# Performance work log

Measured on AMD Instinct MI355X. Metric: run time of the kernel, lower is better.

## Reference

```python
import jax, jax.numpy as jnp
import numpy as np

VOCAB, E, H, OUT = 50000, 300, 512, 256
D = 2 * H  # bidirectional
B, T = 64, 256
EPS = 1e-5


def setup_inputs() -> dict:
    key = jax.random.key(0)
    ks = jax.random.split(key, 16)
    s = 0.05
    inp = {
        'inputs': jax.random.randint(ks[0], (B, T), 0, VOCAB, dtype=jnp.int32),
        'mask': jnp.zeros((B, T), dtype=bool),
        'embed_table': jax.random.normal(ks[1], (VOCAB, E), jnp.float32) * s,
        # forward-direction LSTM (PyTorch gate order i,f,g,o)
        'w_ih_f': jax.random.normal(ks[2], (4 * H, E), jnp.float32) * s,
        'w_hh_f': jax.random.normal(ks[3], (4 * H, H), jnp.float32) * s,
        'b_ih_f': jax.random.normal(ks[4], (4 * H,), jnp.float32) * s,
        'b_hh_f': jax.random.normal(ks[5], (4 * H,), jnp.float32) * s,
        # backward-direction LSTM
        'w_ih_b': jax.random.normal(ks[6], (4 * H, E), jnp.float32) * s,
        'w_hh_b': jax.random.normal(ks[7], (4 * H, H), jnp.float32) * s,
        'b_ih_b': jax.random.normal(ks[8], (4 * H,), jnp.float32) * s,
        'b_hh_b': jax.random.normal(ks[9], (4 * H,), jnp.float32) * s,
        # SoftDotAttention
        'w_in': jax.random.normal(ks[10], (D, D), jnp.float32) * s,       # linear_in, no bias
        'w_out_attn': jax.random.normal(ks[11], (D, 2 * D), jnp.float32) * s,  # linear_out, no bias
        # output head + BatchNorm affine
        'w_out': jax.random.normal(ks[12], (OUT, D), jnp.float32) * s,
        'b_out': jax.random.normal(ks[13], (OUT,), jnp.float32) * s,
        'gamma': jnp.ones((OUT,), jnp.float32),
        'beta': jnp.zeros((OUT,), jnp.float32),
    }
    return inp


def _lstm_dir(x, w_ih, w_hh, b_ih, b_hh, reverse):
    # x: [B, T, E] -> hs: [B, T, H]
    bsz = x.shape[0]
    h0 = jnp.zeros((bsz, w_hh.shape[1]), x.dtype)
    c0 = jnp.zeros_like(h0)
    x_pre = jnp.einsum('bte,ge->btg', x, w_ih) + (b_ih + b_hh)  # precompute input proj

    def cell(carry, xt):
        h, c = carry
        gates = xt + h @ w_hh.T
        i, f, g, o = jnp.split(gates, 4, axis=-1)
        i, f, o = jax.nn.sigmoid(i), jax.nn.sigmoid(f), jax.nn.sigmoid(o)
        g = jnp.tanh(g)
        c = f * c + i * g
        h = o * jnp.tanh(c)
        return (h, c), h

    _, hs = jax.lax.scan(cell, (h0, c0), jnp.swapaxes(x_pre, 0, 1), reverse=reverse)
    return jnp.swapaxes(hs, 0, 1)


def reference(inputs, mask, embed_table, w_ih_f, w_hh_f, b_ih_f, b_hh_f,
              w_ih_b, w_hh_b, b_ih_b, b_hh_b, w_in, w_out_attn,
              w_out, b_out, gamma, beta):
    embeds = embed_table[inputs]                       # [B,T,E]; dropout = identity (eval)
    h_f = _lstm_dir(embeds, w_ih_f, w_hh_f, b_ih_f, b_hh_f, reverse=False)
    h_b = _lstm_dir(embeds, w_ih_b, w_hh_b, b_ih_b, b_hh_b, reverse=True)
    ctx = jnp.concatenate([h_f, h_b], axis=-1)         # [B,T,D]

    # vectorized SoftDotAttention over all query timesteps (the original Python loop)
    target = jnp.einsum('bqd,ed->bqe', ctx, w_in)      # linear_in(ctx[:,q])
    scores = jnp.einsum('bqd,bkd->bqk', target, ctx)   # [B,T,T]
    scores = jnp.where(mask[:, None, :], -jnp.inf, scores)
    attn = jax.nn.softmax(scores, axis=-1)
    weighted = jnp.einsum('bqk,bkd->bqd', attn, ctx)   # [B,T,D]
    h_tilde = jnp.tanh(jnp.einsum('bqc,dc->bqd',
                                  jnp.concatenate([weighted, ctx], axis=-1),
                                  w_out_attn))          # [B,T,D]

    ctx_out = jnp.mean(h_tilde, axis=1)                # [B,D]
    y = jnp.tanh(ctx_out @ w_out.T + b_out)            # [B,OUT]

    # BatchNorm1d, training-mode batch statistics (biased variance)
    mu = jnp.mean(y, axis=0)
    var = jnp.mean((y - mu) ** 2, axis=0)
    out = gamma * (y - mu) * jax.lax.rsqrt(var + EPS) + beta
    return out
```

## Files before the change

### kernel.cpp

```cpp
#include <hip/hip_runtime.h>
#include <hip/hip_fp16.h>

#define NB   64
#define NT   256
#define NE   300
#define NH   512
#define ND   1024
#define NOUT 256

typedef _Float16 f16;
typedef _Float16 f16x4 __attribute__((ext_vector_type(4)));
typedef _Float16 f16x8 __attribute__((ext_vector_type(8)));
typedef float    f32x4 __attribute__((ext_vector_type(4)));

static __device__ __forceinline__ float sigmoidf_(float x) {
  return 1.f / (1.f + __expf(-x));
}
static __device__ __forceinline__ float tanhf_(float x) {
  return 1.f - 2.f / (__expf(2.f * x) + 1.f);
}

template <bool DUAL>
static __device__ __forceinline__ void mfma_tile(
    const f16* __restrict__ A, const f16* __restrict__ A2,
    const f16* __restrict__ B, int K, int Ksplit, int ldA, int ldB,
    int m0, int n0, f32x4 acc[4], f16* As, f16* Bs)
{
  const int tid = threadIdx.x;
  const int lane = tid & 63, w = tid >> 6;
  const int sr = tid >> 2, sk = (tid & 3) * 8;
  const int afr = (w * 16 + (lane & 15)) * 40 + (lane >> 4) * 8;
  for (int kt = 0; kt < K; kt += 32) {
    const f16* Ab = (!DUAL || kt < Ksplit)
        ? (A  + (size_t)(m0 + sr) * ldA + kt + sk)
        : (A2 + (size_t)(m0 + sr) * ldA + (kt - Ksplit) + sk);
    *(f16x8*)&As[sr * 40 + sk] = *(const f16x8*)Ab;
    *(f16x8*)&Bs[sr * 40 + sk] =
        *(const f16x8*)&B[(size_t)(n0 + sr) * ldB + kt + sk];
    __syncthreads();
    f16x8 a = *(const f16x8*)&As[afr];
#pragma unroll
    for (int j = 0; j < 4; ++j) {
      f16x8 b = *(const f16x8*)&Bs[(j * 16 + (lane & 15)) * 40 + (lane >> 4) * 8];
      acc[j] = __builtin_amdgcn_mfma_f32_16x16x32_f16(a, b, acc[j], 0, 0, 0);
    }
    __syncthreads();
  }
}

__global__ __launch_bounds__(256) void gemm_h2h(
    const f16* __restrict__ A, const f16* __restrict__ B, f16* __restrict__ C,
    int N, int K, int sA, int sB, int sC)
{
  __shared__ f16 As[2560], Bs[2560];
  const f16* Ab = A + (size_t)blockIdx.z * sA;
  const f16* Bb = B + (size_t)blockIdx.z * sB;
  f16*       Cb = C + (size_t)blockIdx.z * sC;
  const int m0 = blockIdx.y * 64, n0 = blockIdx.x * 64;
  f32x4 acc[4] = {};
  mfma_tile<false>(Ab, Ab, Bb, K, K, K, K, m0, n0, acc, As, Bs);
  const int lane = threadIdx.x & 63, w = threadIdx.x >> 6;
  const int row = m0 + w * 16 + (lane >> 4) * 4;
  const int col = n0 + (lane & 15);
#pragma unroll
  for (int j = 0; j < 4; ++j)
#pragma unroll
    for (int r = 0; r < 4; ++r)
      Cb[(size_t)(row + r) * N + col + j * 16] = (f16)acc[j][r];
}

__global__ __launch_bounds__(256) void gemm_h2f(
    const f16* __restrict__ A, const f16* __restrict__ B, float* __restrict__ C,
    int N, int K, int sA, int sB, int sC)
{
  __shared__ f16 As[2560], Bs[2560];
  const f16* Ab = A + (size_t)blockIdx.z * sA;
  const f16* Bb = B + (size_t)blockIdx.z * sB;
  float*     Cb = C + (size_t)blockIdx.z * sC;
  const int m0 = blockIdx.y * 64, n0 = blockIdx.x * 64;
  f32x4 acc[4] = {};
  mfma_tile<false>(Ab, Ab, Bb, K, K, K, K, m0, n0, acc, As, Bs);
  const int lane = threadIdx.x & 63, w = threadIdx.x >> 6;
  const int row = m0 + w * 16 + (lane >> 4) * 4;
  const int col = n0 + (lane & 15);
#pragma unroll
  for (int j = 0; j < 4; ++j)
#pragma unroll
    for (int r = 0; r < 4; ++r)
      Cb[(size_t)(row + r) * N + col + j * 16] = acc[j][r];
}

__global__ __launch_bounds__(256) void xpre_mfma(
    const f16* __restrict__ A, const f16* __restrict__ B,
    const float* __restrict__ bihf, const float* __restrict__ bhhf,
    const float* __restrict__ bihb, const float* __restrict__ bhhb,
    f16* __restrict__ xq)
{
  __shared__ __align__(16) f16 As[2560], Bs[2560];
  __shared__ __align__(16) f16 ldsT[64 * 72];
  __shared__ float biasS[64];
  const int ds = blockIdx.x;
  const int dir = ds >> 5, slice = ds & 31;
  const int t0 = blockIdx.y;
  const int tid = threadIdx.x, lane = tid & 63, w = tid >> 6;
  if (tid < 64) {
    int row = dir * 2048 + (tid & 3) * 512 + slice * 16 + (tid >> 2);
    biasS[tid] = (row < 2048) ? (bihf[row] + bhhf[row])
                              : (bihb[row - 2048] + bhhb[row - 2048]);
  }
  const int sr = tid >> 2, sk = (tid & 3) * 8;
  const int brow = dir * 2048 + (sr & 3) * 512 + slice * 16 + (sr >> 2);
  const int afr = (w * 16 + (lane & 15)) * 40 + (lane >> 4) * 8;
  f32x4 acc[4] = {};
  for (int kt = 0; kt < 320; kt += 32) {
    *(f16x8*)&As[sr * 40 + sk] =
        *(const f16x8*)&A[((size_t)(sr * 256 + t0)) * 320 + kt + sk];
    *(f16x8*)&Bs[sr * 40 + sk] =
        *(const f16x8*)&B[((size_t)brow) * 320 + kt + sk];
    __syncthreads();
    f16x8 a = *(const f16x8*)&As[afr];
#pragma unroll
    for (int j = 0; j < 4; ++j) {
      f16x8 b = *(const f16x8*)&Bs[(j * 16 + (lane & 15)) * 40 + (lane >> 4) * 8];
      acc[j] = __builtin_amdgcn_mfma_f32_16x16x32_f16(a, b, acc[j], 0, 0, 0);
    }
    __syncthreads();
  }
#pragma unroll
  for (int j = 0; j < 4; ++j) {
    const int cl = j * 16 + (lane & 15);
#pragma unroll
    for (int r = 0; r < 4; ++r) {
      int b = w * 16 + (lane >> 4) * 4 + r;
      ldsT[b * 72 + cl] = (f16)(acc[j][r] + biasS[cl]);
    }
  }
  __syncthreads();
  f16* base = xq + (((size_t)t0 * 2 + dir) * 32 + slice) * 4096;
#pragma unroll
  for (int p = 0; p < 2; ++p) {
    int e = tid + 256 * p;
    int b = e >> 3, q8 = (e & 7) * 8;
    *(uint4*)(base + b * 64 + q8) = *(const uint4*)&ldsT[b * 72 + q8];
  }
}

__global__ __launch_bounds__(256) void htilde_mfma(
    const f16* __restrict__ Wt, const f16* __restrict__ CTX,
    const f16* __restrict__ Wo, float* __restrict__ ctx_out)
{
  __shared__ f16 As[2560], Bs[2560];
  __shared__ float red[4][64];
  const int m0 = blockIdx.y * 64, n0 = blockIdx.x * 64;
  f32x4 acc[4] = {};
  mfma_tile<true>(Wt, CTX, Wo, 2048, 1024, 1024, 2048, m0, n0, acc, As, Bs);
  const int lane = threadIdx.x & 63, w = threadIdx.x >> 6;
#pragma unroll
  for (int j = 0; j < 4; ++j) {
    float s = 0.f;
#pragma unroll
    for (int r = 0; r < 4; ++r) s += tanhf(acc[j][r]);
    s += __shfl_xor(s, 16, 64);
    s += __shfl_xor(s, 32, 64);
    if (lane < 16) red[w][j * 16 + lane] = s;
  }
  __syncthreads();
  if (threadIdx.x < 64) {
    float s = red[0][threadIdx.x] + red[1][threadIdx.x] +
              red[2][threadIdx.x] + red[3][threadIdx.x];
    int b = m0 >> 8;
    atomicAdd(&ctx_out[(size_t)b * ND + n0 + threadIdx.x], s);
  }
}

__global__ __launch_bounds__(256, 1) void lstm_persist(
    const f16* __restrict__ xq, const float* __restrict__ whhf,
    const float* __restrict__ whhb, f16* __restrict__ hseq)
{
  __shared__ __align__(16) f16 hx[64][24];
  const int blk = blockIdx.x;
  const int dir = blk >> 5;
  const int slice = blk & 31;
  const int j0 = slice * 16;
  const float* whh = dir ? whhb : whhf;
  const int tid = threadIdx.x, lane = tid & 63, w = tid >> 6;
  const int jj = lane & 15, ko = (lane >> 4) * 8;

  f16x8 bf[4][16];
#pragma unroll
  for (int g = 0; g < 4; ++g)
#pragma unroll
    for (int kt = 0; kt < 16; ++kt) {
      const float* src = whh + (size_t)(g * NH + j0 + jj) * NH + kt * 32 + ko;
      float4 u0 = *(const float4*)src;
      float4 u1 = *(const float4*)(src + 4);
      f16x8 v;
      v[0] = (f16)u0.x; v[1] = (f16)u0.y; v[2] = (f16)u0.z; v[3] = (f16)u0.w;
      v[4] = (f16)u1.x; v[5] = (f16)u1.y; v[6] = (f16)u1.z; v[7] = (f16)u1.w;
      bf[g][kt] = v;
    }

  float c[4] = {0.f, 0.f, 0.f, 0.f};
  const int eb = tid >> 2, eg = tid & 3;
  const int aoff = (ko >> 4) * 1024 + (w * 16 + jj) * 16 + (ko & 8);

  float xg[4][4];
  auto ldxg = [&](int t) {
    const int tl = dir ? (NT - 1 - t) : t;
    const f16* base = xq + (((size_t)tl * 2 + dir) * 32 + slice) * 4096;
#pragma unroll
    for (int r = 0; r < 4; ++r) {
      const int b = w * 16 + (lane >> 4) * 4 + r;
      unsigned long long u = *(const unsigned long long*)(base + b * 64 + jj * 4);
      f16x4 x = __builtin_bit_cast(f16x4, u);
      xg[0][r] = (float)x[0];
      xg[1][r] = (float)x[1];
      xg[2][r] = (float)x[2];
      xg[3][r] = (float)x[3];
    }
  };
  ldxg(0);

  unsigned long long u0[16], u1[16];

  for (int t = 0; t < NT; ++t) {
    const int tt = dir ? (NT - 1 - t) : t;

    f32x4 acc[4] = {};
    if (t > 0) {
      const int ttp = dir ? (NT - t) : (t - 1);
      const f16* hp = hseq + ((size_t)ttp * 2 + dir) * 32768 + aoff;
      for (;;) {
        int nb = 0;
#pragma unroll
        for (int kt = 0; kt < 16; ++kt) {
          nb |= (unsigned)(u0[kt] >> 48) == 0xFFFFu;
          nb |= (unsigned)(u1[kt] >> 48) == 0xFFFFu;
        }
        if (!__any(nb)) break;
#pragma unroll
        for (int kt = 0; kt < 16; ++kt) {
          if ((unsigned)(u0[kt] >> 48) == 0xFFFFu)
            u0[kt] = __hip_atomic_load(
                (const unsigned long long*)(hp + kt * 2048),
                __ATOMIC_RELAXED, __HIP_MEMORY_SCOPE_AGENT);
          if ((unsigned)(u1[kt] >> 48) == 0xFFFFu)
            u1[kt] = __hip_atomic_load(
                (const unsigned long long*)(hp + kt * 2048 + 4),
                __ATOMIC_RELAXED, __HIP_MEMORY_SCOPE_AGENT);
        }
      }
#pragma unroll
      for (int kt = 0; kt < 16; ++kt) {
        f16x4 a0 = __builtin_bit_cast(f16x4, u0[kt]);
        f16x4 a1 = __builtin_bit_cast(f16x4, u1[kt]);
        f16x8 a = __builtin_shufflevector(a0, a1, 0, 1, 2, 3, 4, 5, 6, 7);
#pragma unroll
        for (int g = 0; g < 4; ++g)
          acc[g] = __builtin_amdgcn_mfma_f32_16x16x32_f16(a, bf[g][kt], acc[g], 0, 0, 0);
      }
    }
#pragma unroll
    for (int r = 0; r < 4; ++r) {
      float iv = sigmoidf_(acc[0][r] + xg[0][r]);
      float fv = sigmoidf_(acc[1][r] + xg[1][r]);
      float gv = tanhf_   (acc[2][r] + xg[2][r]);
      float ov = sigmoidf_(acc[3][r] + xg[3][r]);
      c[r] = fv * c[r] + iv * gv;
      float h = ov * tanhf_(c[r]);
      hx[w * 16 + (lane >> 4) * 4 + r][jj] = (f16)h;
    }
    asm volatile("s_waitcnt lgkmcnt(0)" ::: "memory");
    __builtin_amdgcn_sched_barrier(0);
    f16x4 hv = *(const f16x4*)&hx[eb][eg * 4];
    unsigned long long pu = __builtin_bit_cast(unsigned long long, hv);
    __hip_atomic_store(
        (unsigned long long*)(hseq + ((size_t)tt * 2 + dir) * 32768
                              + (size_t)slice * 1024 + eb * 16 + eg * 4),
        pu, __ATOMIC_RELAXED, __HIP_MEMORY_SCOPE_AGENT);
    if (t == NT - 1) break;
    {
      const f16* hn = hseq + ((size_t)tt * 2 + dir) * 32768 + aoff;
#pragma unroll
      for (int kt = 0; kt < 16; ++kt) {
        u0[kt] = __hip_atomic_load(
            (const unsigned long long*)(hn + kt * 2048),
            __ATOMIC_RELAXED, __HIP_MEMORY_SCOPE_AGENT);
        u1[kt] = __hip_atomic_load(
            (const unsigned long long*)(hn + kt * 2048 + 4),
            __ATOMIC_RELAXED, __HIP_MEMORY_SCOPE_AGENT);
      }
    }
    ldxg(t + 1);
  }
}

__global__ __launch_bounds__(256) void fill_sent(unsigned long long* __restrict__ p)
{
  size_t i = (size_t)blockIdx.x * 1024 + threadIdx.x;
#pragma unroll
  for (int k = 0; k < 4; ++k)
    __hip_atomic_store(p + i + k * 256, 0xFFFFFFFFFFFFFFFFull,
                       __ATOMIC_RELAXED, __HIP_MEMORY_SCOPE_AGENT);
}

__global__ __launch_bounds__(256) void tr_k(
    const f16* __restrict__ hseq, f16* __restrict__ ctx, f16* __restrict__ ctxT)
{
  __shared__ __align__(16) f16 X[4][64][72];
  const int t0 = blockIdx.x * 64;
  const int dir = blockIdx.y;
  const int bg = blockIdx.z;
  const int tid = threadIdx.x;
  for (int ci = 0; ci < 8; ++ci) {
#pragma unroll
    for (int p = 0; p < 8; ++p) {
      int q = tid + 256 * p;
      int ti = q >> 5, rem = q & 31;
      int si = rem >> 3, s2 = rem & 7;
      int bi = s2 >> 1, jjh = (s2 & 1) * 8;
      const f16* src = hseq
          + (((size_t)(t0 + ti) * 2 + dir) * 32 + ci * 4 + si) * 1024
          + (bg * 4 + bi) * 16 + jjh;
      *(uint4*)&X[bi][ti][si * 16 + jjh] = *(const uint4*)src;
    }
    __syncthreads();
#pragma unroll
    for (int p = 0; p < 8; ++p) {
      int q = tid + 256 * p;
      int bi = q >> 9, rem = q & 511;
      int ti = rem >> 3, sub = (rem & 7) * 8;
      f16* dst = ctx + ((size_t)(bg * 4 + bi) * NT + t0 + ti) * ND
                 + dir * 512 + ci * 64 + sub;
      *(uint4*)dst = *(const uint4*)&X[bi][ti][sub];
    }
#pragma unroll
    for (int p = 0; p < 8; ++p) {
      int q = tid + 256 * p;
      int bi = q >> 9, rem = q & 511;
      int dl = rem >> 3, ts = (rem & 7) * 8;
      f16x8 v;
#pragma unroll
      for (int k = 0; k < 8; ++k) v[k] = X[bi][ts + k][dl];
      f16* dst = ctxT + ((size_t)(bg * 4 + bi) * ND + dir * 512 + ci * 64 + dl) * NT
                 + t0 + ts;
      *(f16x8*)dst = v;
    }
    __syncthreads();
  }
}

__global__ __launch_bounds__(256) void softmax_rows(
    const float* __restrict__ sc, f16* __restrict__ probs)
{
  const int row = blockIdx.x * 4 + (threadIdx.x >> 6);
  const int lane = threadIdx.x & 63;
  const float* p = sc + (size_t)row * NT;
  float4 v = *(const float4*)&p[lane * 4];
  float mx = fmaxf(fmaxf(v.x, v.y), fmaxf(v.z, v.w));
#pragma unroll
  for (int s = 32; s >= 1; s >>= 1) mx = fmaxf(mx, __shfl_xor(mx, s, 64));
  v.x = __expf(v.x - mx); v.y = __expf(v.y - mx);
  v.z = __expf(v.z - mx); v.w = __expf(v.w - mx);
  float sm = v.x + v.y + v.z + v.w;
#pragma unroll
  for (int s = 32; s >= 1; s >>= 1) sm += __shfl_xor(sm, s, 64);
  float inv = 1.f / sm;
  f16* q = probs + (size_t)row * NT + lane * 4;
  q[0] = (f16)(v.x * inv); q[1] = (f16)(v.y * inv);
  q[2] = (f16)(v.z * inv); q[3] = (f16)(v.w * inv);
}

__global__ __launch_bounds__(256) void head_k(
    const float* __restrict__ ctx_out, const float* __restrict__ w_out,
    const float* __restrict__ b_out, float* __restrict__ y)
{
  const int b = blockIdx.x;
  __shared__ float cl[ND];
#pragma unroll
  for (int l = 0; l < 4; ++l)
    cl[threadIdx.x + 256 * l] =
        ctx_out[(size_t)b * ND + threadIdx.x + 256 * l] * (1.f / (float)NT);
  __syncthreads();
  const int n = threadIdx.x;
  float acc = b_out[n];
  for (int k = 0; k < ND; k += 4) {
    float4 w = *(const float4*)&w_out[(size_t)n * ND + k];
    acc += cl[k] * w.x + cl[k + 1] * w.y + cl[k + 2] * w.z + cl[k + 3] * w.w;
  }
  y[b * NOUT + n] = tanhf(acc);
}

__global__ __launch_bounds__(64) void bn_k(
    const float* __restrict__ y, const float* __restrict__ gamma,
    const float* __restrict__ beta, float* __restrict__ out)
{
  const int n = blockIdx.x, b = threadIdx.x;
  float v = y[b * NOUT + n];
  float s = v, sq = v * v;
#pragma unroll
  for (int k = 32; k >= 1; k >>= 1) {
    s  += __shfl_xor(s, k, 64);
    sq += __shfl_xor(sq, k, 64);
  }
  float mu = s * (1.f / 64.f);
  float var = sq * (1.f / 64.f) - mu * mu;
  float r = rsqrtf(var + 1e-5f);
  out[b * NOUT + n] = gamma[n] * (v - mu) * r + beta[n];
}

__global__ __launch_bounds__(256) void zero_k(float4* __restrict__ p, int n4)
{
  int i = blockIdx.x * 256 + threadIdx.x;
  if (i < n4) p[i] = make_float4(0.f, 0.f, 0.f, 0.f);
}

__global__ __launch_bounds__(256) void gather_emb(
    const int* __restrict__ toks, const float* __restrict__ table,
    f16* __restrict__ emb)
{
  const int w = threadIdx.x >> 6, lane = threadIdx.x & 63;
  const int row = blockIdx.x * 4 + w;
  const int tok = toks[row];
  for (int k = lane; k < 320; k += 64)
    emb[(size_t)row * 320 + k] = (k < NE) ? (f16)table[(size_t)tok * NE + k]
                                          : (f16)0.f;
}

__global__ __launch_bounds__(256) void cvt_wih(
    const float* __restrict__ wf, const float* __restrict__ wb,
    f16* __restrict__ o)
{
  const int row = blockIdx.x;
  const float* src = (row < 2048) ? (wf + (size_t)row * NE)
                                  : (wb + (size_t)(row - 2048) * NE);
  for (int k = threadIdx.x; k < 320; k += 256)
    o[(size_t)row * 320 + k] = (k < NE) ? (f16)src[k] : (f16)0.f;
}

__global__ __launch_bounds__(256) void cvt_flat(
    const float* __restrict__ in, f16* __restrict__ o, int n)
{
  int i = blockIdx.x * 256 + threadIdx.x;
  if (i < n) o[i] = (f16)in[i];
}

extern "C" void kernel_launch(void* const* d_in, const int* in_sizes, int n_in,
                              void* d_out, int out_size, void* d_ws,
                              size_t ws_size, hipStream_t stream)
{
  (void)in_sizes; (void)n_in; (void)out_size;
  const int*   inputs  = (const int*)d_in[0];
  const float* table   = (const float*)d_in[2];
  const float* w_ih_f  = (const float*)d_in[3];
  const float* w_hh_f  = (const float*)d_in[4];
  const float* b_ih_f  = (const float*)d_in[5];
  const float* b_hh_f  = (const float*)d_in[6];
  const float* w_ih_b  = (const float*)d_in[7];
  const float* w_hh_b  = (const float*)d_in[8];
  const float* b_ih_b  = (const float*)d_in[9];
  const float* b_hh_b  = (const float*)d_in[10];
  const float* w_in    = (const float*)d_in[11];
  const float* w_oattn = (const float*)d_in[12];
  const float* w_out   = (const float*)d_in[13];
  const float* b_out   = (const float*)d_in[14];
  const float* gamma   = (const float*)d_in[15];
  const float* beta    = (const float*)d_in[16];

  char* ws = (char*)d_ws;
  f16*   xq      = (f16*)ws;
  f16*   ctxT_h  = (f16*)ws;
  f16*   tw_h    = (f16*)(ws + 33554432);
  float* scores  = (float*)(ws + 67108864);
  f16*   probs   = (f16*)(ws + 83886080);
  f16*   w_in_h  = (f16*)(ws + 92274688);
  f16*   ctx_h   = (f16*)(ws + 134217728);
  f16*   hseq    = (f16*)(ws + 167772160);
  f16*   emb_h   = (f16*)(ws + 201326592);
  float* ctxout  = (float*)(ws + 201588736);
  float* yb      = (float*)(ws + 201850880);
  f16*   wih_h   = (f16*)(ws + 211812352);
  f16*   w_oattn_h = (f16*)(ws + 214433792);
  if (ws_size < 218628096ULL) return;

  gather_emb<<<4096, 256, 0, stream>>>(inputs, table, emb_h);
  cvt_wih<<<4096, 256, 0, stream>>>(w_ih_f, w_ih_b, wih_h);
  cvt_flat<<<8192, 256, 0, stream>>>(w_oattn, w_oattn_h, 2097152);

  fill_sent<<<4096, 256, 0, stream>>>((unsigned long long*)hseq);

  xpre_mfma<<<dim3(64, 256), 256, 0, stream>>>(
      emb_h, wih_h, b_ih_f, b_hh_f, b_ih_b, b_hh_b, xq);

  zero_k<<<82, 256, 0, stream>>>((float4*)ctxout, 20992);
  lstm_persist<<<64, 256, 0, stream>>>(xq, w_hh_f, w_hh_b, hseq);

  tr_k<<<dim3(4, 2, 16), 256, 0, stream>>>(hseq, ctx_h, ctxT_h);

  cvt_flat<<<4096, 256, 0, stream>>>(w_in, w_in_h, 1048576);
  gemm_h2h<<<dim3(16, 256, 1), 256, 0, stream>>>(
      ctx_h, w_in_h, tw_h, ND, ND, 0, 0, 0);

  gemm_h2f<<<dim3(4, 4, NB), 256, 0, stream>>>(
      tw_h, ctx_h, scores, NT, ND, NT * ND, NT * ND, NT * NT);

  softmax_rows<<<(NB * NT) / 4, 256, 0, stream>>>(scores, probs);

  gemm_h2h<<<dim3(16, 4, NB), 256, 0, stream>>>(
      probs, ctxT_h, tw_h, ND, NT, NT * NT, ND * NT, NT * ND);

  htilde_mfma<<<dim3(16, 256), 256, 0, stream>>>(tw_h, ctx_h, w_oattn_h, ctxout);

  head_k<<<NB, 256, 0, stream>>>(ctxout, w_out, b_out, yb);

  bn_k<<<NOUT, 64, 0, stream>>>(yb, gamma, beta, (float*)d_out);
}
```

Before: 1.713 ms.

## Use 128-bit sc1 loads/stores and per-tile incremental MFMA in LSTM recurrence polling

The cross-block exchange of LSTM hidden states now uses 16-byte inline-asm global loads and stores with the sc1 cache bit, replacing pairs of 8-byte relaxed atomic loads and 8-byte atomic stores. The spin-wait no longer waits for the whole h vector before computing. It tracks which k-tiles have arrived (sentinel-checked across the wave) and issues their MFMAs at once, re-polling only the missing tiles. The intent is to cut latency on the serial timestep critical path by overlapping compute with waiting and halving memory transactions. It adds a __syncthreads, and it relies on 16-byte stores being seen atomically, since the sentinel is checked only in the high halves of the .y and .w words.

Measured after the change: 1.826 ms. +6.6%, slower.

```diff
diff --git a/kernel.cpp b/kernel.cpp
--- a/kernel.cpp
+++ b/kernel.cpp
@@ -201,7 +201,7 @@
     }
 
   float c[4] = {0.f, 0.f, 0.f, 0.f};
-  const int eb = tid >> 2, eg = tid & 3;
+  const int eb2 = tid >> 1, eh = (tid & 1) * 8;
   const int aoff = (ko >> 4) * 1024 + (w * 16 + jj) * 16 + (ko & 8);
 
   float xg[4][4];
@@ -221,7 +221,7 @@
   };
   ldxg(0);
 
-  unsigned long long u0[16], u1[16];
+  uint4 U[16];
 
   for (int t = 0; t < NT; ++t) {
     const int tt = dir ? (NT - 1 - t) : t;
@@ -230,34 +230,37 @@
     if (t > 0) {
       const int ttp = dir ? (NT - t) : (t - 1);
       const f16* hp = hseq + ((size_t)ttp * 2 + dir) * 32768 + aoff;
-      for (;;) {
-        int nb = 0;
-#pragma unroll
-        for (int kt = 0; kt < 16; ++kt) {
-          nb |= (unsigned)(u0[kt] >> 48) == 0xFFFFu;
-          nb |= (unsigned)(u1[kt] >> 48) == 0xFFFFu;
+      asm volatile("s_waitcnt vmcnt(0)" ::: "memory");
+      __builtin_amdgcn_sched_barrier(0);
+      unsigned rem = 0xFFFFu;
+      while (rem) {
+        unsigned newly = 0;
+#pragma unroll
+        for (int kt = 0; kt < 16; ++kt)
+          if (rem & (1u << kt)) {
+            int ok = ((U[kt].y >> 16) != 0xFFFFu) &
+                     ((U[kt].w >> 16) != 0xFFFFu);
+            if (__all(ok)) newly |= 1u << kt;
+          }
+#pragma unroll
+        for (int kt = 0; kt < 16; ++kt)
+          if (newly & (1u << kt)) {
+            f16x8 a = __builtin_bit_cast(f16x8, U[kt]);
+#pragma unroll
+            for (int g = 0; g < 4; ++g)
+              acc[g] = __builtin_amdgcn_mfma_f32_16x16x32_f16(
+                  a, bf[g][kt], acc[g], 0, 0, 0);
+          }
+        rem &= ~newly;
+        if (rem) {
+#pragma unroll
+          for (int kt = 0; kt < 16; ++kt)
+            if (rem & (1u << kt))
+              asm volatile("global_load_dwordx4 %0, %1, off sc1"
+                           : "=v"(U[kt]) : "v"(hp + kt * 2048) : "memory");
+          asm volatile("s_waitcnt vmcnt(0)" ::: "memory");
+          __builtin_amdgcn_sched_barrier(0);
         }
-        if (!__any(nb)) break;
-#pragma unroll
-        for (int kt = 0; kt < 16; ++kt) {
-          if ((unsigned)(u0[kt] >> 48) == 0xFFFFu)
-            u0[kt] = __hip_atomic_load(
-                (const unsigned long long*)(hp + kt * 2048),
-                __ATOMIC_RELAXED, __HIP_MEMORY_SCOPE_AGENT);
-          if ((unsigned)(u1[kt] >> 48) == 0xFFFFu)
-            u1[kt] = __hip_atomic_load(
-                (const unsigned long long*)(hp + kt * 2048 + 4),
-                __ATOMIC_RELAXED, __HIP_MEMORY_SCOPE_AGENT);
-        }
-      }
-#pragma unroll
-      for (int kt = 0; kt < 16; ++kt) {
-        f16x4 a0 = __builtin_bit_cast(f16x4, u0[kt]);
-        f16x4 a1 = __builtin_bit_cast(f16x4, u1[kt]);
-        f16x8 a = __builtin_shufflevector(a0, a1, 0, 1, 2, 3, 4, 5, 6, 7);
-#pragma unroll
-        for (int g = 0; g < 4; ++g)
-          acc[g] = __builtin_amdgcn_mfma_f32_16x16x32_f16(a, bf[g][kt], acc[g], 0, 0, 0);
       }
     }
 #pragma unroll
@@ -270,26 +273,21 @@
       float h = ov * tanhf_(c[r]);
       hx[w * 16 + (lane >> 4) * 4 + r][jj] = (f16)h;
     }
-    asm volatile("s_waitcnt lgkmcnt(0)" ::: "memory");
-    __builtin_amdgcn_sched_barrier(0);
-    f16x4 hv = *(const f16x4*)&hx[eb][eg * 4];
-    unsigned long long pu = __builtin_bit_cast(unsigned long long, hv);
-    __hip_atomic_store(
-        (unsigned long long*)(hseq + ((size_t)tt * 2 + dir) * 32768
-                              + (size_t)slice * 1024 + eb * 16 + eg * 4),
-        pu, __ATOMIC_RELAXED, __HIP_MEMORY_SCOPE_AGENT);
+    __syncthreads();
+    if (tid < 128) {
+      f16x8 hv = *(const f16x8*)&hx[eb2][eh];
+      const f16* dst = hseq + ((size_t)tt * 2 + dir) * 32768
+                       + (size_t)slice * 1024 + eb2 * 16 + eh;
+      asm volatile("global_store_dwordx4 %0, %1, off sc1"
+                   :: "v"(dst), "v"(hv) : "memory");
+    }
     if (t == NT - 1) break;
     {
       const f16* hn = hseq + ((size_t)tt * 2 + dir) * 32768 + aoff;
 #pragma unroll
-      for (int kt = 0; kt < 16; ++kt) {
-        u0[kt] = __hip_atomic_load(
-            (const unsigned long long*)(hn + kt * 2048),
-            __ATOMIC_RELAXED, __HIP_MEMORY_SCOPE_AGENT);
-        u1[kt] = __hip_atomic_load(
-            (const unsigned long long*)(hn + kt * 2048 + 4),
-            __ATOMIC_RELAXED, __HIP_MEMORY_SCOPE_AGENT);
-      }
+      for (int kt = 0; kt < 16; ++kt)
+        asm volatile("global_load_dwordx4 %0, %1, off sc1"
+                     : "=v"(U[kt]) : "v"(hn + kt * 2048) : "memory");
     }
     ldxg(t + 1);
   }
```
